# Performance work log

Hardware: AMD Instinct MI355X
Metric: run time of the kernel (lower is better)

## Reference

```python
import jax, jax.numpy as jnp
import numpy as np

B, T, H = 4, 512, 512          # batch, num_target_nodes, hidden
V = 32000                       # static vocab
S, SDV = 512, 300               # source nodes, source dynamic vocab
TDV = 512                       # target dynamic vocab


def setup_inputs() -> dict:
    key = jax.random.key(0)
    ks = jax.random.split(key, 9)
    src_idx = jax.random.randint(ks[6], (B, S), 0, SDV)
    tgt_idx = jax.random.randint(ks[8], (B, T), 0, TDV)
    return {
        "hiddens": jax.random.normal(ks[0], (B, T, H), jnp.float32),
        "Wp": jax.random.normal(ks[1], (H, 3), jnp.float32) * (1.0 / np.sqrt(H)),
        "bp": jnp.zeros((3,), jnp.float32),
        "Wv": jax.random.normal(ks[2], (H, V), jnp.float32) * (1.0 / np.sqrt(H)),
        "bv": jnp.zeros((V,), jnp.float32),
        "source_attentions": jax.nn.softmax(jax.random.normal(ks[3], (B, T, S), jnp.float32), axis=-1),
        "source_attention_maps": jax.nn.one_hot(src_idx, SDV, dtype=jnp.float32),
        "target_attentions": jax.nn.softmax(jax.random.normal(ks[4], (B, T, TDV), jnp.float32), axis=-1),
        "target_attention_maps": jax.nn.one_hot(tgt_idx, TDV, dtype=jnp.float32),
    }


def reference(hiddens, Wp, bp, Wv, bv, source_attentions, source_attention_maps,
              target_attentions, target_attention_maps):
    b, t, h = hiddens.shape
    hf = hiddens.reshape(b * t, h)
    # switch probabilities: [copy_source, copy_target, generate]
    p = jax.nn.softmax(hf @ Wp + bp, axis=1).reshape(b, t, 3)
    p_copy_source = p[..., 0:1]
    p_copy_target = p[..., 1:2]
    p_generate = p[..., 2:3]
    # vocab scores with pad index masked to -inf (vocab_pad_idx = 0)
    scores = hf @ Wv + bv                      # [b*t, V]
    scores = scores.at[:, 0].set(-jnp.inf)
    vocab_probs = jax.nn.softmax(scores.reshape(b, t, -1), axis=-1)
    scaled_vocab_probs = vocab_probs * p_generate
    # copy distributions via one-hot scatter-sum (dense matmul in original)
    scaled_copy_source_probs = jnp.einsum(
        'bts,bsv->btv', source_attentions * p_copy_source, source_attention_maps)
    scaled_copy_target_probs = jnp.einsum(
        'btn,bnv->btv', target_attentions * p_copy_target, target_attention_maps)
    probs = jnp.concatenate(
        [scaled_vocab_probs, scaled_copy_source_probs, scaled_copy_target_probs], axis=2)
    predictions = jnp.argmax(probs, axis=2)
    return (probs, predictions)
```

## Files before the change

### kernel.cpp

```cpp
#include <hip/hip_runtime.h>
#include <hip/hip_bf16.h>
#include <math.h>

#define Bq   4
#define Tq   512
#define Hq   512
#define Vq   32000
#define Sq   512
#define SDVq 300
#define TDVq 512
#define ROWS (Bq * Tq)
#define OUTW (Vq + SDVq + TDVq)

typedef __bf16 bf16x8 __attribute__((ext_vector_type(8)));
typedef float  fx4    __attribute__((ext_vector_type(4)));

__device__ __forceinline__ void async16(const void* g, void* l) {
    __builtin_amdgcn_global_load_lds(
        (const __attribute__((address_space(1))) void*)g,
        (__attribute__((address_space(3))) void*)l, 16, 0, 0);
}

__global__ void compute_p(const float* __restrict__ hiddens,
                          const float* __restrict__ Wp,
                          const float* __restrict__ bp,
                          float* __restrict__ p) {
    int row  = blockIdx.x;
    int lane = threadIdx.x;
    const float* h = hiddens + (size_t)row * Hq;
    float a0 = 0.f, a1 = 0.f, a2 = 0.f;
    for (int i = lane; i < Hq; i += 64) {
        float hv = h[i];
        a0 += hv * Wp[i * 3 + 0];
        a1 += hv * Wp[i * 3 + 1];
        a2 += hv * Wp[i * 3 + 2];
    }
    for (int off = 32; off > 0; off >>= 1) {
        a0 += __shfl_down(a0, off);
        a1 += __shfl_down(a1, off);
        a2 += __shfl_down(a2, off);
    }
    if (lane == 0) {
        float l0 = a0 + bp[0], l1 = a1 + bp[1], l2 = a2 + bp[2];
        float M  = fmaxf(l0, fmaxf(l1, l2));
        float e0 = expf(l0 - M), e1 = expf(l1 - M), e2 = expf(l2 - M);
        float inv = 1.f / (e0 + e1 + e2);
        p[row * 3 + 0] = e0 * inv;
        p[row * 3 + 1] = e1 * inv;
        p[row * 3 + 2] = e2 * inv;
    }
}

__global__ void extract_idx(const float* __restrict__ map, int ncols,
                            int* __restrict__ idx) {
    int row  = blockIdx.x;
    int lane = threadIdx.x;
    const float* r = map + (size_t)row * ncols;
    float best = -1.f; int bi = 0;
    for (int i = lane; i < ncols; i += 64) {
        float v = r[i];
        if (v > best) { best = v; bi = i; }
    }
    for (int off = 32; off > 0; off >>= 1) {
        float ob  = __shfl_down(best, off);
        int   obi = __shfl_down(bi, off);
        if (ob > best) { best = ob; bi = obi; }
    }
    if (lane == 0) idx[row] = bi;
}

__global__ __launch_bounds__(256)
void convert_a(const float* __restrict__ in, __hip_bfloat16* __restrict__ o) {
    int i = blockIdx.x * 256 + threadIdx.x;
    float4 v = ((const float4*)in)[i];
    __hip_bfloat16* op = o + (size_t)i * 4;
    op[0] = __float2bfloat16(v.x);
    op[1] = __float2bfloat16(v.y);
    op[2] = __float2bfloat16(v.z);
    op[3] = __float2bfloat16(v.w);
}

__global__ __launch_bounds__(256)
void transpose_wv(const float* __restrict__ Wv, __hip_bfloat16* __restrict__ Wt) {
    __shared__ float t[32][33];
    int n0 = blockIdx.x * 32, k0 = blockIdx.y * 32;
    int tx = threadIdx.x, ty = threadIdx.y;
#pragma unroll
    for (int r = 0; r < 4; ++r)
        t[ty + r * 8][tx] = Wv[(size_t)(k0 + ty + r * 8) * Vq + n0 + tx];
    __syncthreads();
#pragma unroll
    for (int r = 0; r < 4; ++r)
        Wt[(size_t)(n0 + ty + r * 8) * Hq + k0 + tx] =
            __float2bfloat16(t[tx][ty + r * 8]);
}

__global__ __launch_bounds__(256)
void gemm_mfma(const __hip_bfloat16* __restrict__ A,
               const __hip_bfloat16* __restrict__ Bt,
               const float* __restrict__ bv,
               float* __restrict__ out) {
    __shared__ __align__(16) unsigned short As[4096];
    __shared__ __align__(16) unsigned short Bs[4096];
    int tid  = threadIdx.x;
    int wave = tid >> 6, lane = tid & 63;
    int bm = blockIdx.x * 128;
    int bn = blockIdx.y * 128;
    int wr = wave >> 1, wc = wave & 1;
    int lr = lane & 15;
    int kq = lane >> 4;

    fx4 acc[4][4];
#pragma unroll
    for (int i = 0; i < 4; ++i)
#pragma unroll
        for (int j = 0; j < 4; ++j)
            acc[i][j] = (fx4){0.f, 0.f, 0.f, 0.f};

    int c0 = tid, c1 = tid + 256;
    int ar0 = c0 & 127, ak0 = (c0 >> 7) * 8;
    int ar1 = c1 & 127, ak1 = (c1 >> 7) * 8;
    const unsigned short* Ag = (const unsigned short*)A;
    const unsigned short* Bg = (const unsigned short*)Bt;
    unsigned short* As0 = &As[(wave << 6) * 8];
    unsigned short* As1 = &As[(256 + (wave << 6)) * 8];
    unsigned short* Bs0 = &Bs[(wave << 6) * 8];
    unsigned short* Bs1 = &Bs[(256 + (wave << 6)) * 8];

    for (int k0 = 0; k0 < Hq; k0 += 32) {
        async16(Ag + (size_t)(bm + ar0) * Hq + k0 + ak0, As0);
        async16(Ag + (size_t)(bm + ar1) * Hq + k0 + ak1, As1);
        async16(Bg + (size_t)(bn + ar0) * Hq + k0 + ak0, Bs0);
        async16(Bg + (size_t)(bn + ar1) * Hq + k0 + ak1, Bs1);
        __syncthreads();

        bf16x8 af[4], bfr[4];
#pragma unroll
        for (int i = 0; i < 4; ++i) {
            int row = wr * 64 + i * 16 + lr;
            af[i] = *(const bf16x8*)&As[(size_t)(kq * 128 + row) * 8];
        }
#pragma unroll
        for (int j = 0; j < 4; ++j) {
            int col = wc * 64 + j * 16 + lr;
            bfr[j] = *(const bf16x8*)&Bs[(size_t)(kq * 128 + col) * 8];
        }
#pragma unroll
        for (int i = 0; i < 4; ++i)
#pragma unroll
            for (int j = 0; j < 4; ++j)
                acc[i][j] = __builtin_amdgcn_mfma_f32_16x16x32_bf16(
                    af[i], bfr[j], acc[i][j], 0, 0, 0);
        __syncthreads();
    }

    float bvv[4];
#pragma unroll
    for (int j = 0; j < 4; ++j)
        bvv[j] = bv[bn + wc * 64 + j * 16 + lr];
#pragma unroll
    for (int i = 0; i < 4; ++i) {
        int gr0 = bm + wr * 64 + i * 16 + kq * 4;
#pragma unroll
        for (int j = 0; j < 4; ++j) {
            int gc = bn + wc * 64 + j * 16 + lr;
#pragma unroll
            for (int r = 0; r < 4; ++r) {
                float v = acc[i][j][r] + bvv[j];
                if (gc == 0) v = -1e30f;
                out[(size_t)(gr0 + r) * OUTW + gc] = v;
            }
        }
    }
}

__global__ __launch_bounds__(256)
void softmax_rows(float* __restrict__ out, const float* __restrict__ p,
                  float* __restrict__ cval, int* __restrict__ cidx) {
    int row = blockIdx.x;
    int tid = threadIdx.x;
    float* rp = out + (size_t)row * OUTW;
    const float4* rv = (const float4*)rp;

    float m = -INFINITY, l = 0.f; int mi = 0;
    for (int i = tid; i < Vq / 4; i += 256) {
        float4 v = rv[i];
        float vv[4] = {v.x, v.y, v.z, v.w};
#pragma unroll
        for (int c = 0; c < 4; ++c) {
            float x = vv[c];
            if (x > m) { l = l * __expf(m - x) + 1.f; m = x; mi = i * 4 + c; }
            else       { l += __expf(x - m); }
        }
    }
    __shared__ float sm[256], sl[256];
    __shared__ int   si[256];
    sm[tid] = m; sl[tid] = l; si[tid] = mi;
    __syncthreads();
    for (int s = 128; s > 0; s >>= 1) {
        if (tid < s) {
            float m1 = sm[tid], l1 = sl[tid]; int i1 = si[tid];
            float m2 = sm[tid + s], l2 = sl[tid + s]; int i2 = si[tid + s];
            float M = fmaxf(m1, m2);
            sl[tid] = l1 * __expf(m1 - M) + l2 * __expf(m2 - M);
            sm[tid] = M;
            si[tid] = (m2 > m1 || (m2 == m1 && i2 < i1)) ? i2 : i1;
        }
        __syncthreads();
    }
    float M = sm[0], L = sl[0];
    float pgen = p[row * 3 + 2];
    float scale = pgen / L;
    if (tid == 0) { cval[row * 3] = scale; cidx[row * 3] = si[0]; }

    float4* wv4 = (float4*)rp;
    for (int i = tid; i < Vq / 4; i += 256) {
        float4 v = rv[i];
        v.x = __expf(v.x - M) * scale;
        v.y = __expf(v.y - M) * scale;
        v.z = __expf(v.z - M) * scale;
        v.w = __expf(v.w - M) * scale;
        wv4[i] = v;
    }
}

__global__ __launch_bounds__(256)
void copy_scatter(const float* __restrict__ att, const int* __restrict__ idx,
                  const float* __restrict__ p, int pcol, int slot,
                  int natt, int nout, float* __restrict__ out, int out_off,
                  float* __restrict__ cval, int* __restrict__ cidx) {
    int row = blockIdx.x;
    int b   = row >> 9;
    int tid = threadIdx.x;
    __shared__ float acc[TDVq];
    for (int i = tid; i < nout; i += 256) acc[i] = 0.f;
    __syncthreads();
    const float* arow = att + (size_t)row * natt;
    const int*   ib   = idx + b * natt;
    for (int s = tid; s < natt; s += 256) {
        atomicAdd(&acc[ib[s]], arow[s]);
    }
    __syncthreads();
    float pc = p[row * 3 + pcol];
    float* orow = out + (size_t)row * OUTW + out_off;
    float bm_ = -INFINITY; int bi = 0;
    for (int v = tid; v < nout; v += 256) {
        float val = acc[v] * pc;
        orow[v] = val;
        if (val > bm_) { bm_ = val; bi = v; }
    }
    __shared__ float bs[256];
    __shared__ int   is_[256];
    bs[tid] = bm_; is_[tid] = bi;
    __syncthreads();
    for (int s = 128; s > 0; s >>= 1) {
        if (tid < s) {
            float v2 = bs[tid + s]; int i2 = is_[tid + s];
            if (v2 > bs[tid] || (v2 == bs[tid] && i2 < is_[tid])) {
                bs[tid] = v2; is_[tid] = i2;
            }
        }
        __syncthreads();
    }
    if (tid == 0) { cval[row * 3 + slot] = bs[0]; cidx[row * 3 + slot] = out_off + is_[0]; }
}

__global__ void combine_pred(const float* __restrict__ cval,
                             const int* __restrict__ cidx,
                             float* __restrict__ pred) {
    int r = blockIdx.x * 256 + threadIdx.x;
    if (r >= ROWS) return;
    float v = cval[r * 3]; int i = cidx[r * 3];
    if (cval[r * 3 + 1] > v) { v = cval[r * 3 + 1]; i = cidx[r * 3 + 1]; }
    if (cval[r * 3 + 2] > v) { v = cval[r * 3 + 2]; i = cidx[r * 3 + 2]; }
    pred[r] = (float)i;
}

extern "C" void kernel_launch(void* const* d_in, const int* in_sizes, int n_in,
                              void* d_out, int out_size, void* d_ws, size_t ws_size,
                              hipStream_t stream) {
    const float* hiddens = (const float*)d_in[0];
    const float* Wp      = (const float*)d_in[1];
    const float* bp      = (const float*)d_in[2];
    const float* Wv      = (const float*)d_in[3];
    const float* bv      = (const float*)d_in[4];
    const float* src_att = (const float*)d_in[5];
    const float* src_map = (const float*)d_in[6];
    const float* tgt_att = (const float*)d_in[7];
    const float* tgt_map = (const float*)d_in[8];

    float* out  = (float*)d_out;
    float* pred = out + (size_t)ROWS * OUTW;

    char* ws = (char*)d_ws;
    float* p_ws   = (float*)(ws);
    int*   sidx   = (int*)(ws + (24 << 10));
    int*   tidx   = (int*)(ws + (32 << 10));
    float* cval   = (float*)(ws + (40 << 10));
    int*   cidx   = (int*)(ws + (64 << 10));
    __hip_bfloat16* A_bf = (__hip_bfloat16*)(ws + (128 << 10));
    __hip_bfloat16* Wt   = (__hip_bfloat16*)(ws + (128 << 10) + (2 << 20));

    convert_a<<<ROWS * Hq / 4 / 256, 256, 0, stream>>>(hiddens, A_bf);
    {
        dim3 tg(Vq / 32, Hq / 32);
        dim3 tb(32, 8);
        transpose_wv<<<tg, tb, 0, stream>>>(Wv, Wt);
    }

    compute_p<<<ROWS, 64, 0, stream>>>(hiddens, Wp, bp, p_ws);
    extract_idx<<<Bq * Sq, 64, 0, stream>>>(src_map, SDVq, sidx);
    extract_idx<<<Bq * Tq, 64, 0, stream>>>(tgt_map, TDVq, tidx);

    {
        dim3 gg(ROWS / 128, Vq / 128);
        gemm_mfma<<<gg, 256, 0, stream>>>(A_bf, Wt, bv, out);
    }

    softmax_rows<<<ROWS, 256, 0, stream>>>(out, p_ws, cval, cidx);

    copy_scatter<<<ROWS, 256, 0, stream>>>(src_att, sidx, p_ws, 0, 1, Sq, SDVq,
                                           out, Vq, cval, cidx);
    copy_scatter<<<ROWS, 256, 0, stream>>>(tgt_att, tidx, p_ws, 1, 2, TDVq, TDVq,
                                           out, Vq + SDVq, cval, cidx);

    combine_pred<<<(ROWS + 255) / 256, 256, 0, stream>>>(cval, cidx, pred);
}
```

Baseline: 652.7 us.

## Fuse exp and row-sum into GEMM epilogue and triple-buffer K loads

The GEMM epilogue now writes exp(logit) directly and accumulates per-row sums through shared and global atomics. That replaces the two-pass online-softmax kernel with a single scale-and-argmax pass over the vocab. The K loop is also rewritten as a 3-stage async global-to-LDS pipeline with explicit vmcnt waits, so loads overlap with MFMA work. The exp is taken without subtracting a max, which risks overflow for large logits and relies on the inputs keeping logits small. The triple buffers also use more LDS per block, which may reduce occupancy.

```diff
diff --git a/kernel.cpp b/kernel.cpp
--- a/kernel.cpp
+++ b/kernel.cpp
@@ -24,9 +24,11 @@
 __global__ void compute_p(const float* __restrict__ hiddens,
                           const float* __restrict__ Wp,
                           const float* __restrict__ bp,
-                          float* __restrict__ p) {
+                          float* __restrict__ p,
+                          float* __restrict__ rowsum) {
     int row  = blockIdx.x;
     int lane = threadIdx.x;
+    if (lane == 0) rowsum[row] = 0.f;
     const float* h = hiddens + (size_t)row * Hq;
     float a0 = 0.f, a1 = 0.f, a2 = 0.f;
     for (int i = lane; i < Hq; i += 64) {
@@ -99,9 +101,11 @@
 void gemm_mfma(const __hip_bfloat16* __restrict__ A,
                const __hip_bfloat16* __restrict__ Bt,
                const float* __restrict__ bv,
-               float* __restrict__ out) {
-    __shared__ __align__(16) unsigned short As[4096];
-    __shared__ __align__(16) unsigned short Bs[4096];
+               float* __restrict__ out,
+               float* __restrict__ rowsum) {
+    __shared__ __align__(16) unsigned short As[3 * 4096];
+    __shared__ __align__(16) unsigned short Bs[3 * 4096];
+    __shared__ float rs[128];
     int tid  = threadIdx.x;
     int wave = tid >> 6, lane = tid & 63;
     int bm = blockIdx.x * 128;
@@ -122,106 +126,124 @@
     int ar1 = c1 & 127, ak1 = (c1 >> 7) * 8;
     const unsigned short* Ag = (const unsigned short*)A;
     const unsigned short* Bg = (const unsigned short*)Bt;
-    unsigned short* As0 = &As[(wave << 6) * 8];
-    unsigned short* As1 = &As[(256 + (wave << 6)) * 8];
-    unsigned short* Bs0 = &Bs[(wave << 6) * 8];
-    unsigned short* Bs1 = &Bs[(256 + (wave << 6)) * 8];
-
-    for (int k0 = 0; k0 < Hq; k0 += 32) {
-        async16(Ag + (size_t)(bm + ar0) * Hq + k0 + ak0, As0);
-        async16(Ag + (size_t)(bm + ar1) * Hq + k0 + ak1, As1);
-        async16(Bg + (size_t)(bn + ar0) * Hq + k0 + ak0, Bs0);
-        async16(Bg + (size_t)(bn + ar1) * Hq + k0 + ak1, Bs1);
-        __syncthreads();
-
+
+#define STAGE(tt, bb) do {                                                   \
+        int k0s = (tt) * 32;                                                 \
+        unsigned short* Ab = &As[(bb) * 4096 + (wave << 6) * 8];             \
+        unsigned short* Bb = &Bs[(bb) * 4096 + (wave << 6) * 8];             \
+        async16(Ag + (size_t)(bm + ar0) * Hq + k0s + ak0, Ab);               \
+        async16(Ag + (size_t)(bm + ar1) * Hq + k0s + ak1, Ab + 2048);        \
+        async16(Bg + (size_t)(bn + ar0) * Hq + k0s + ak0, Bb);               \
+        async16(Bg + (size_t)(bn + ar1) * Hq + k0s + ak1, Bb + 2048);        \
+    } while (0)
+
+    STAGE(0, 0);
+    STAGE(1, 1);
+
+#pragma unroll
+    for (int t = 0; t < 16; ++t) {
+        if (t < 15) asm volatile("s_waitcnt vmcnt(4)" ::: "memory");
+        else        asm volatile("s_waitcnt vmcnt(0)" ::: "memory");
+        __builtin_amdgcn_s_barrier();
+        asm volatile("" ::: "memory");
+
+        const unsigned short* Asb = &As[(t % 3) * 4096];
+        const unsigned short* Bsb = &Bs[(t % 3) * 4096];
         bf16x8 af[4], bfr[4];
 #pragma unroll
-        for (int i = 0; i < 4; ++i) {
-            int row = wr * 64 + i * 16 + lr;
-            af[i] = *(const bf16x8*)&As[(size_t)(kq * 128 + row) * 8];
-        }
-#pragma unroll
-        for (int j = 0; j < 4; ++j) {
-            int col = wc * 64 + j * 16 + lr;
-            bfr[j] = *(const bf16x8*)&Bs[(size_t)(kq * 128 + col) * 8];
-        }
+        for (int i = 0; i < 4; ++i)
+            af[i] = *(const bf16x8*)&Asb[(size_t)(kq * 128 + wr * 64 + i * 16 + lr) * 8];
+#pragma unroll
+        for (int j = 0; j < 4; ++j)
+            bfr[j] = *(const bf16x8*)&Bsb[(size_t)(kq * 128 + wc * 64 + j * 16 + lr) * 8];
+
+        if (t + 2 < 16) STAGE(t + 2, (t + 2) % 3);
+
 #pragma unroll
         for (int i = 0; i < 4; ++i)
 #pragma unroll
             for (int j = 0; j < 4; ++j)
                 acc[i][j] = __builtin_amdgcn_mfma_f32_16x16x32_bf16(
                     af[i], bfr[j], acc[i][j], 0, 0, 0);
-        __syncthreads();
-    }
+
+        asm volatile("s_waitcnt lgkmcnt(0)" ::: "memory");
+    }
+#undef STAGE
+
+    if (tid < 128) rs[tid] = 0.f;
+    __syncthreads();
 
     float bvv[4];
 #pragma unroll
     for (int j = 0; j < 4; ++j)
         bvv[j] = bv[bn + wc * 64 + j * 16 + lr];
+
 #pragma unroll
     for (int i = 0; i < 4; ++i) {
-        int gr0 = bm + wr * 64 + i * 16 + kq * 4;
+        int lrow = wr * 64 + i * 16 + kq * 4;
+        float rsum[4] = {0.f, 0.f, 0.f, 0.f};
 #pragma unroll
         for (int j = 0; j < 4; ++j) {
             int gc = bn + wc * 64 + j * 16 + lr;
 #pragma unroll
             for (int r = 0; r < 4; ++r) {
-                float v = acc[i][j][r] + bvv[j];
-                if (gc == 0) v = -1e30f;
-                out[(size_t)(gr0 + r) * OUTW + gc] = v;
+                float v = __expf(acc[i][j][r] + bvv[j]);
+                if (gc == 0) v = 0.f;
+                out[(size_t)(bm + lrow + r) * OUTW + gc] = v;
+                rsum[r] += v;
             }
         }
-    }
-}
-
-__global__ __launch_bounds__(256)
-void softmax_rows(float* __restrict__ out, const float* __restrict__ p,
-                  float* __restrict__ cval, int* __restrict__ cidx) {
+#pragma unroll
+        for (int off = 1; off < 16; off <<= 1) {
+#pragma unroll
+            for (int r = 0; r < 4; ++r)
+                rsum[r] += __shfl_xor(rsum[r], off);
+        }
+        if (lr == 0) {
+#pragma unroll
+            for (int r = 0; r < 4; ++r)
+                atomicAdd(&rs[lrow + r], rsum[r]);
+        }
+    }
+    __syncthreads();
+    if (tid < 128) atomicAdd(&rowsum[bm + tid], rs[tid]);
+}
+
+__global__ __launch_bounds__(256)
+void scale_rows(float* __restrict__ out, const float* __restrict__ rowsum,
+                const float* __restrict__ p,
+                float* __restrict__ cval, int* __restrict__ cidx) {
     int row = blockIdx.x;
     int tid = threadIdx.x;
     float* rp = out + (size_t)row * OUTW;
+    float scale = p[row * 3 + 2] / rowsum[row];
+
     const float4* rv = (const float4*)rp;
-
-    float m = -INFINITY, l = 0.f; int mi = 0;
+    float4* wv = (float4*)rp;
+    float bm_ = -1.f; int bi = 0;
     for (int i = tid; i < Vq / 4; i += 256) {
         float4 v = rv[i];
-        float vv[4] = {v.x, v.y, v.z, v.w};
-#pragma unroll
-        for (int c = 0; c < 4; ++c) {
-            float x = vv[c];
-            if (x > m) { l = l * __expf(m - x) + 1.f; m = x; mi = i * 4 + c; }
-            else       { l += __expf(x - m); }
-        }
-    }
-    __shared__ float sm[256], sl[256];
-    __shared__ int   si[256];
-    sm[tid] = m; sl[tid] = l; si[tid] = mi;
+        if (v.x > bm_) { bm_ = v.x; bi = i * 4 + 0; }
+        if (v.y > bm_) { bm_ = v.y; bi = i * 4 + 1; }
+        if (v.z > bm_) { bm_ = v.z; bi = i * 4 + 2; }
+        if (v.w > bm_) { bm_ = v.w; bi = i * 4 + 3; }
+        v.x *= scale; v.y *= scale; v.z *= scale; v.w *= scale;
+        wv[i] = v;
+    }
+    __shared__ float bs[256];
+    __shared__ int   is_[256];
+    bs[tid] = bm_; is_[tid] = bi;
     __syncthreads();
     for (int s = 128; s > 0; s >>= 1) {
         if (tid < s) {
-            float m1 = sm[tid], l1 = sl[tid]; int i1 = si[tid];
-            float m2 = sm[tid + s], l2 = sl[tid + s]; int i2 = si[tid + s];
-            float M = fmaxf(m1, m2);
-            sl[tid] = l1 * __expf(m1 - M) + l2 * __expf(m2 - M);
-            sm[tid] = M;
-            si[tid] = (m2 > m1 || (m2 == m1 && i2 < i1)) ? i2 : i1;
+            float v2 = bs[tid + s]; int i2 = is_[tid + s];
+            if (v2 > bs[tid] || (v2 == bs[tid] && i2 < is_[tid])) {
+                bs[tid] = v2; is_[tid] = i2;
+            }
         }
         __syncthreads();
     }
-    float M = sm[0], L = sl[0];
-    float pgen = p[row * 3 + 2];
-    float scale = pgen / L;
-    if (tid == 0) { cval[row * 3] = scale; cidx[row * 3] = si[0]; }
-
-    float4* wv4 = (float4*)rp;
-    for (int i = tid; i < Vq / 4; i += 256) {
-        float4 v = rv[i];
-        v.x = __expf(v.x - M) * scale;
-        v.y = __expf(v.y - M) * scale;
-        v.z = __expf(v.z - M) * scale;
-        v.w = __expf(v.w - M) * scale;
-        wv4[i] = v;
-    }
+    if (tid == 0) { cval[row * 3] = bs[0] * scale; cidx[row * 3] = is_[0]; }
 }
 
 __global__ __launch_bounds__(256)
@@ -298,6 +320,7 @@
     int*   tidx   = (int*)(ws + (32 << 10));
     float* cval   = (float*)(ws + (40 << 10));
     int*   cidx   = (int*)(ws + (64 << 10));
+    float* rowsum = (float*)(ws + (88 << 10));
     __hip_bfloat16* A_bf = (__hip_bfloat16*)(ws + (128 << 10));
     __hip_bfloat16* Wt   = (__hip_bfloat16*)(ws + (128 << 10) + (2 << 20));
 
@@ -308,16 +331,16 @@
         transpose_wv<<<tg, tb, 0, stream>>>(Wv, Wt);
     }
 
-    compute_p<<<ROWS, 64, 0, stream>>>(hiddens, Wp, bp, p_ws);
+    compute_p<<<ROWS, 64, 0, stream>>>(hiddens, Wp, bp, p_ws, rowsum);
     extract_idx<<<Bq * Sq, 64, 0, stream>>>(src_map, SDVq, sidx);
     extract_idx<<<Bq * Tq, 64, 0, stream>>>(tgt_map, TDVq, tidx);
 
     {
         dim3 gg(ROWS / 128, Vq / 128);
-        gemm_mfma<<<gg, 256, 0, stream>>>(A_bf, Wt, bv, out);
-    }
-
-    softmax_rows<<<ROWS, 256, 0, stream>>>(out, p_ws, cval, cidx);
+        gemm_mfma<<<gg, 256, 0, stream>>>(A_bf, Wt, bv, out, rowsum);
+    }
+
+    scale_rows<<<ROWS, 256, 0, stream>>>(out, rowsum, p_ws, cval, cidx);
 
     copy_scatter<<<ROWS, 256, 0, stream>>>(src_att, sidx, p_ws, 0, 1, Sq, SDVq,
                                            out, Vq, cval, cidx);
```

Result: faster. 620.2 us (-5.0%).
